# Optimization experiments

Measured on AMD Instinct MI355X. Metric: run time of the kernel, lower is better.

The kernel has to match this reference:

```python
import jax, jax.numpy as jnp
import numpy as np

B, C, H, W = 32, 64, 128, 128
N_KNOTS = 65
GRID = 0.125  # spline_grid_from_range(65, 4.0) = (4.0/32)//1e-6*1e-6 = 0.125


def setup_inputs() -> dict:
    key = jax.random.key(0)
    k1, k2 = jax.random.split(key)
    x = jax.random.normal(k1, (B, C, H, W), dtype=jnp.float32) * 2.0
    coefficients_vect = jax.random.normal(k2, (C * N_KNOTS,), dtype=jnp.float32)
    grid = jnp.float32(GRID)
    zero_knot_indexes = jnp.arange(C, dtype=jnp.int32) * N_KNOTS + N_KNOTS // 2
    return {
        "x": x,
        "coefficients_vect": coefficients_vect,
        "grid": grid,
        "zero_knot_indexes": zero_knot_indexes,
        "size": N_KNOTS,
    }


def reference(x, coefficients_vect, grid, zero_knot_indexes, size):
    half = size // 2
    # clamp so that indexes, indexes+1, indexes+2 stay inside the per-channel table
    x_clamped = jnp.clip(x, -grid * half, grid * (half - 2))
    floored_x = jnp.floor(x_clamped / grid)
    # per-element knot index into flattened (C, n_knots) table
    indexes = (zero_knot_indexes.reshape(1, -1, 1, 1) + floored_x).astype(jnp.int32)
    # fractional position within the knot interval (uses unclamped x, as in torch)
    shift1 = (x - floored_x * grid) / grid
    frac1 = (shift1 - 1) ** 2 / 2
    frac2 = (-2 * shift1**2 + 2 * shift1 + 1) / 2
    frac3 = shift1**2 / 2
    c0 = coefficients_vect[indexes]
    c1 = coefficients_vect[indexes + 1]
    c2 = coefficients_vect[indexes + 2]
    return c2 * frac3 + c1 * frac2 + c0 * frac1
```

## Files before the change

kernel.cpp:

```cpp
#include <hip/hip_runtime.h>


typedef float vfloat4 __attribute__((ext_vector_type(4)));

__global__ __launch_bounds__(256) void quad_spline_kernel(
    const vfloat4* __restrict__ x,
    const float*   __restrict__ coeffs,
    const float*   __restrict__ grid_p,
    const int*     __restrict__ zki,
    const int*     __restrict__ size_p,
    vfloat4*       __restrict__ out)
{
    __shared__ vfloat4 lds_a[63];

    const int tid   = threadIdx.x;
    const int vbase = blockIdx.x * 1024 + tid;
    const int c     = (blockIdx.x >> 2) & 63;

    vfloat4 x0 = x[vbase];
    vfloat4 x1 = x[vbase + 256];
    vfloat4 x2 = x[vbase + 512];
    vfloat4 x3 = x[vbase + 768];

    const float g    = grid_p[0];
    const int   size = size_p[0];
    const int   half = size >> 1;
    const int   base = zki[c] - half;

    if (tid < 63) {
        float c0 = coeffs[base + tid];
        float c1 = coeffs[base + tid + 1];
        float c2 = coeffs[base + tid + 2];
        vfloat4 a;
        a.x = 0.5f * (c0 + c1);
        a.y = c1 - c0;
        a.z = 0.5f * ((c0 - c1) + (c2 - c1));
        a.w = 0.0f;
        lds_a[tid] = a;
    }
    __syncthreads();

    const float inv_g = 1.0f / g;
    const float flo   = -(float)half;
    const float fhi   =  (float)(half - 2);

    #define SPLINE(xx, dst)                                            \
    {                                                                  \
        float t   = (xx) * inv_g;                                      \
        float fl  = fminf(fmaxf(floorf(t), flo), fhi);                 \
        int   idx = half + (int)fl;                                    \
        float s   = t - fl;                                            \
        vfloat4 a = lds_a[idx];                                        \
        (dst) = fmaf(s, fmaf(s, a.z, a.y), a.x);                       \
    }

    vfloat4 r0, r1, r2, r3;
    SPLINE(x0.x, r0.x) SPLINE(x0.y, r0.y) SPLINE(x0.z, r0.z) SPLINE(x0.w, r0.w)
    SPLINE(x1.x, r1.x) SPLINE(x1.y, r1.y) SPLINE(x1.z, r1.z) SPLINE(x1.w, r1.w)
    SPLINE(x2.x, r2.x) SPLINE(x2.y, r2.y) SPLINE(x2.z, r2.z) SPLINE(x2.w, r2.w)
    SPLINE(x3.x, r3.x) SPLINE(x3.y, r3.y) SPLINE(x3.z, r3.z) SPLINE(x3.w, r3.w)
    #undef SPLINE

    out[vbase]       = r0;
    out[vbase + 256] = r1;
    out[vbase + 512] = r2;
    out[vbase + 768] = r3;
}

extern "C" void kernel_launch(void* const* d_in, const int* in_sizes, int n_in,
                              void* d_out, int out_size, void* d_ws, size_t ws_size,
                              hipStream_t stream) {
    const vfloat4* x      = (const vfloat4*)d_in[0];
    const float*   coeffs = (const float*)d_in[1];
    const float*   grid_p = (const float*)d_in[2];
    const int*     zki    = (const int*)d_in[3];
    const int*     size_p = (const int*)d_in[4];
    vfloat4*       out    = (vfloat4*)d_out;

    const int n4     = in_sizes[0] / 4;
    const int blocks = n4 / 1024;

    quad_spline_kernel<<<blocks, 256, 0, stream>>>(x, coeffs, grid_p, zki, size_p, out);
}
```

Measured before the change: 236.4 us.

## Process a full channel slice per block with double-buffered nontemporal loads

```diff
diff --git a/kernel.cpp b/kernel.cpp
--- a/kernel.cpp
+++ b/kernel.cpp
@@ -14,13 +14,9 @@
     __shared__ vfloat4 lds_a[63];
 
     const int tid   = threadIdx.x;
-    const int vbase = blockIdx.x * 1024 + tid;
-    const int c     = (blockIdx.x >> 2) & 63;
-
-    vfloat4 x0 = x[vbase];
-    vfloat4 x1 = x[vbase + 256];
-    vfloat4 x2 = x[vbase + 512];
-    vfloat4 x3 = x[vbase + 768];
+    const int slice = blockIdx.x;
+    const int c     = slice & 63;
+    const int vbase = slice * 4096 + tid;
 
     const float g    = grid_p[0];
     const int   size = size_p[0];
@@ -54,17 +50,50 @@
         (dst) = fmaf(s, fmaf(s, a.z, a.y), a.x);                       \
     }
 
-    vfloat4 r0, r1, r2, r3;
-    SPLINE(x0.x, r0.x) SPLINE(x0.y, r0.y) SPLINE(x0.z, r0.z) SPLINE(x0.w, r0.w)
-    SPLINE(x1.x, r1.x) SPLINE(x1.y, r1.y) SPLINE(x1.z, r1.z) SPLINE(x1.w, r1.w)
-    SPLINE(x2.x, r2.x) SPLINE(x2.y, r2.y) SPLINE(x2.z, r2.z) SPLINE(x2.w, r2.w)
-    SPLINE(x3.x, r3.x) SPLINE(x3.y, r3.y) SPLINE(x3.z, r3.z) SPLINE(x3.w, r3.w)
+    #define COMPUTE4(xv0, xv1, xv2, xv3, off)                          \
+    {                                                                  \
+        vfloat4 r0, r1, r2, r3;                                        \
+        SPLINE(xv0.x, r0.x) SPLINE(xv0.y, r0.y)                        \
+        SPLINE(xv0.z, r0.z) SPLINE(xv0.w, r0.w)                        \
+        SPLINE(xv1.x, r1.x) SPLINE(xv1.y, r1.y)                        \
+        SPLINE(xv1.z, r1.z) SPLINE(xv1.w, r1.w)                        \
+        SPLINE(xv2.x, r2.x) SPLINE(xv2.y, r2.y)                        \
+        SPLINE(xv2.z, r2.z) SPLINE(xv2.w, r2.w)                        \
+        SPLINE(xv3.x, r3.x) SPLINE(xv3.y, r3.y)                        \
+        SPLINE(xv3.z, r3.z) SPLINE(xv3.w, r3.w)                        \
+        __builtin_nontemporal_store(r0, &out[(off)]);                  \
+        __builtin_nontemporal_store(r1, &out[(off) + 256]);            \
+        __builtin_nontemporal_store(r2, &out[(off) + 512]);            \
+        __builtin_nontemporal_store(r3, &out[(off) + 768]);            \
+    }
+
+    vfloat4 xa0 = __builtin_nontemporal_load(&x[vbase]);
+    vfloat4 xa1 = __builtin_nontemporal_load(&x[vbase + 256]);
+    vfloat4 xa2 = __builtin_nontemporal_load(&x[vbase + 512]);
+    vfloat4 xa3 = __builtin_nontemporal_load(&x[vbase + 768]);
+
+    vfloat4 xb0 = __builtin_nontemporal_load(&x[vbase + 1024]);
+    vfloat4 xb1 = __builtin_nontemporal_load(&x[vbase + 1280]);
+    vfloat4 xb2 = __builtin_nontemporal_load(&x[vbase + 1536]);
+    vfloat4 xb3 = __builtin_nontemporal_load(&x[vbase + 1792]);
+
+    COMPUTE4(xa0, xa1, xa2, xa3, vbase);
+    xa0 = __builtin_nontemporal_load(&x[vbase + 2048]);
+    xa1 = __builtin_nontemporal_load(&x[vbase + 2304]);
+    xa2 = __builtin_nontemporal_load(&x[vbase + 2560]);
+    xa3 = __builtin_nontemporal_load(&x[vbase + 2816]);
+
+    COMPUTE4(xb0, xb1, xb2, xb3, vbase + 1024);
+    xb0 = __builtin_nontemporal_load(&x[vbase + 3072]);
+    xb1 = __builtin_nontemporal_load(&x[vbase + 3328]);
+    xb2 = __builtin_nontemporal_load(&x[vbase + 3584]);
+    xb3 = __builtin_nontemporal_load(&x[vbase + 3840]);
+
+    COMPUTE4(xa0, xa1, xa2, xa3, vbase + 2048);
+    COMPUTE4(xb0, xb1, xb2, xb3, vbase + 3072);
+
+    #undef COMPUTE4
     #undef SPLINE
-
-    out[vbase]       = r0;
-    out[vbase + 256] = r1;
-    out[vbase + 512] = r2;
-    out[vbase + 768] = r3;
 }
 
 extern "C" void kernel_launch(void* const* d_in, const int* in_sizes, int n_in,
@@ -78,7 +107,7 @@
     vfloat4*       out    = (vfloat4*)d_out;
 
     const int n4     = in_sizes[0] / 4;
-    const int blocks = n4 / 1024;
+    const int blocks = n4 / 4096;
 
     quad_spline_kernel<<<blocks, 256, 0, stream>>>(x, coeffs, grid_p, zki, size_p, out);
 }
```

Measured after the change: 230.4 us. -2.6%, faster.
